# Kernel tuning notes

Hardware: AMD Instinct MI355X
Metric: run time of the kernel (lower is better)

Reference implementation:

```python
import jax, jax.numpy as jnp
import numpy as np

NUM_EXPERTS = 8
TOP_K = 2
N_EMBD = 1024
SEQ = 2048
BATCH = 1
BLOCK = 128
D_FFN = ((4 * N_EMBD // TOP_K) + BLOCK - 1) // BLOCK * BLOCK  # 2048


def setup_inputs() -> dict:
    key = jax.random.key(0)
    k_x, k_r, k_w1, k_w2 = jax.random.split(key, 4)
    x = jax.random.normal(k_x, (BATCH, SEQ, N_EMBD), dtype=jnp.float32)
    # nn.Linear(n_embd, num_experts, bias=False) -> weight [E, D]
    w_router = jax.random.normal(k_r, (NUM_EXPERTS, N_EMBD), dtype=jnp.float32) * 0.02
    # trunc_normal std=0.02 approximated by clipped normal
    w1 = jnp.clip(jax.random.normal(k_w1, (N_EMBD, D_FFN * NUM_EXPERTS), dtype=jnp.float32) * 0.02, -0.06, 0.06)
    w2 = jnp.clip(jax.random.normal(k_w2, (D_FFN * NUM_EXPERTS, N_EMBD), dtype=jnp.float32) * 0.02, -0.06, 0.06)
    return {"x": x, "w_router": w_router, "w1": w1, "w2": w2}


def reference(x, w_router, w1, w2):
    B, S, D = x.shape
    E = w_router.shape[0]
    d_ffn = w1.shape[1] // E
    xf = x.reshape(-1, D)                      # [N, D]
    N = xf.shape[0]

    # --- routing (softmax in fp32, top-k, renormalize) ---
    logits = xf @ w_router.T                   # [N, E]
    probs = jax.nn.softmax(logits.astype(jnp.float32), axis=-1)
    topw, sel = jax.lax.top_k(probs, TOP_K)    # [N, k]
    topw = topw / jnp.sum(topw, axis=-1, keepdims=True)
    topw = topw.astype(x.dtype)

    # dense per-token gate matrix [N, E]; zero for unselected experts, so the
    # dense grouped-GEMM below computes exactly the routed-expert math.
    gates = jnp.zeros((N, E), dtype=x.dtype).at[jnp.arange(N)[:, None], sel].set(topw)

    w1r = w1.reshape(D, E, d_ffn)              # expert e uses columns e*d_ffn:(e+1)*d_ffn
    w2r = w2.reshape(E, d_ffn, D)

    out = jnp.zeros_like(xf)
    for e in range(E):                         # small fixed expert count
        h = jax.nn.gelu(xf @ w1r[:, e, :], approximate=False)  # torch F.gelu = exact erf
        out = out + gates[:, e:e + 1] * (h @ w2r[e])
    return out.reshape(B, S, D)
```

## Files before the change

kernel.cpp:

```cpp
#include <hip/hip_runtime.h>

typedef short bf16x8 __attribute__((ext_vector_type(8)));
typedef float f32x4 __attribute__((ext_vector_type(4)));
typedef unsigned short u16;
typedef unsigned int u32;

#define N_TOK 2048
#define D_EMB 1024
#define D_FFNC 2048
#define N_EXP 8

__device__ __forceinline__ u16 f2bf(float f) {
    u32 u = __builtin_bit_cast(u32, f);
    u32 r = (u + 0x7fffu + ((u >> 16) & 1u)) >> 16;
    return (u16)r;
}

__device__ __forceinline__ void gl_lds16(const void* g, void* l) {
    __builtin_amdgcn_global_load_lds((const __attribute__((address_space(1))) u32*)g,
                                     (__attribute__((address_space(3))) u32*)l, 16, 0, 0);
}

__global__ __launch_bounds__(256) void k_router(const float* __restrict__ x,
                                                const float* __restrict__ wr,
                                                u16* __restrict__ xb,
                                                int* __restrict__ eids,
                                                float* __restrict__ gate2) {
    int lane = threadIdx.x & 63;
    int wv = threadIdx.x >> 6;
    int t = blockIdx.x * 4 + wv;
    const float* xp = x + (size_t)t * D_EMB;
    float p[N_EXP];
#pragma unroll
    for (int e = 0; e < N_EXP; e++) p[e] = 0.f;
#pragma unroll
    for (int i = 0; i < 4; i++) {
        int idx = (i * 64 + lane) * 4;
        float4 v = *reinterpret_cast<const float4*>(xp + idx);
        ushort4 o;
        o.x = f2bf(v.x); o.y = f2bf(v.y); o.z = f2bf(v.z); o.w = f2bf(v.w);
        *reinterpret_cast<ushort4*>(xb + (size_t)t * D_EMB + idx) = o;
#pragma unroll
        for (int e = 0; e < N_EXP; e++) {
            float4 w = *reinterpret_cast<const float4*>(wr + e * D_EMB + idx);
            p[e] += v.x * w.x + v.y * w.y + v.z * w.z + v.w * w.w;
        }
    }
#pragma unroll
    for (int off = 32; off; off >>= 1) {
#pragma unroll
        for (int e = 0; e < N_EXP; e++) p[e] += __shfl_xor(p[e], off);
    }
    float mx = p[0];
#pragma unroll
    for (int e = 1; e < N_EXP; e++) mx = fmaxf(mx, p[e]);
    float pr[N_EXP];
#pragma unroll
    for (int e = 0; e < N_EXP; e++) pr[e] = expf(p[e] - mx);
    int e1 = 0; float v1 = pr[0];
#pragma unroll
    for (int e = 1; e < N_EXP; e++) { if (pr[e] > v1) { v1 = pr[e]; e1 = e; } }
    int e2 = -1; float v2 = -1.f;
#pragma unroll
    for (int e = 0; e < N_EXP; e++) { if (e != e1 && pr[e] > v2) { v2 = pr[e]; e2 = e; } }
    if (lane == 0) {
        float inv = 1.f / (v1 + v2);
        eids[t * 2] = e1; eids[t * 2 + 1] = e2;
        gate2[t * 2] = v1 * inv; gate2[t * 2 + 1] = v2 * inv;
    }
}

__global__ __launch_bounds__(256) void k_transpose(const float* __restrict__ in,
                                                   u16* __restrict__ out, int R, int C) {
    __shared__ float tl[64][65];
    int c0 = blockIdx.x * 64, r0 = blockIdx.y * 64;
    int tid = threadIdx.x;
    int rr = tid >> 4, c4 = (tid & 15) * 4;
#pragma unroll
    for (int i = 0; i < 4; i++) {
        int r = rr + i * 16;
        float4 v = *reinterpret_cast<const float4*>(in + (size_t)(r0 + r) * C + c0 + c4);
        tl[r][c4] = v.x; tl[r][c4 + 1] = v.y; tl[r][c4 + 2] = v.z; tl[r][c4 + 3] = v.w;
    }
    __syncthreads();
    int k4 = (tid & 15) * 4;
#pragma unroll
    for (int i = 0; i < 4; i++) {
        int cc = rr + i * 16;
        ushort4 o;
        o.x = f2bf(tl[k4][cc]); o.y = f2bf(tl[k4 + 1][cc]);
        o.z = f2bf(tl[k4 + 2][cc]); o.w = f2bf(tl[k4 + 3][cc]);
        *reinterpret_cast<ushort4*>(out + (size_t)(c0 + cc) * R + r0 + k4) = o;
    }
}

__global__ __launch_bounds__(256) void k_build(const int* __restrict__ eids,
                                               const float* __restrict__ gate2,
                                               int* __restrict__ cnt, int* __restrict__ basep,
                                               int* __restrict__ rowmeta, float* __restrict__ rowgate) {
    __shared__ int scnt[8], sbase[8], sfill[8];
    int tid = threadIdx.x;
    if (tid < 8) { scnt[tid] = 0; sfill[tid] = 0; }
    __syncthreads();
    for (int t = tid; t < N_TOK; t += 256) {
        atomicAdd(&scnt[eids[2 * t]], 1);
        atomicAdd(&scnt[eids[2 * t + 1]], 1);
    }
    __syncthreads();
    if (tid == 0) { int s = 0; for (int e = 0; e < 8; e++) { sbase[e] = s; s += scnt[e]; } }
    __syncthreads();
    if (tid < 8) { cnt[tid] = scnt[tid]; basep[tid] = sbase[tid]; }
    for (int t = tid; t < N_TOK; t += 256) {
#pragma unroll
        for (int s = 0; s < 2; s++) {
            int e = eids[2 * t + s];
            int pos = atomicAdd(&sfill[e], 1);
            int g = sbase[e] + pos;
            rowmeta[g] = t | (s << 16);
            rowgate[g] = gate2[2 * t + s];
        }
    }
}

__global__ __launch_bounds__(256) void k_gemm1(const u16* __restrict__ xb,
                                               const u16* __restrict__ w1t,
                                               const int* __restrict__ cnt,
                                               const int* __restrict__ basep,
                                               const int* __restrict__ rowmeta,
                                               u16* __restrict__ hbuf) {
    int e = blockIdx.z;
    int nrows = cnt[e];
    int mt = blockIdx.x, nt = blockIdx.y;
    if (mt * 128 >= nrows) return;
    int b0 = basep[e];
    __shared__ u16 lA[128 * 64];
    __shared__ u16 lB[128 * 64];
    int tid = threadIdx.x, lane = tid & 63, wv = tid >> 6;
    int srow8 = lane >> 3;
    int c8 = lane & 7;
    int csw = (c8 ^ srow8) * 16;
    const char* xbB = (const char*)xb;
    const char* w1tB = (const char*)w1t;
    size_t asrc[4], bsrc[4];
    u16 *adst[4], *bdst[4];
#pragma unroll
    for (int i = 0; i < 4; i++) {
        int r = wv * 32 + i * 8 + srow8;
        int g = mt * 128 + r;
        int tok = (g < nrows) ? (rowmeta[b0 + g] & 0xffff) : (rowmeta[b0] & 0xffff);
        asrc[i] = (size_t)tok * 2048 + csw;
        int colg = nt * 128 + r;
        bsrc[i] = (size_t)(e * 2048 + colg) * 2048 + csw;
        adst[i] = lA + (wv * 32 + i * 8) * 64;
        bdst[i] = lB + (wv * 32 + i * 8) * 64;
    }
    f32x4 acc[4][4];
#pragma unroll
    for (int m = 0; m < 4; m++)
#pragma unroll
        for (int n = 0; n < 4; n++) acc[m][n] = (f32x4){0.f, 0.f, 0.f, 0.f};
    int wr = (wv >> 1) * 64, wc = (wv & 1) * 64;
    int lr = lane & 15, kg = lane >> 4;
#pragma unroll
    for (int i = 0; i < 4; i++) { gl_lds16(xbB + asrc[i], adst[i]); gl_lds16(w1tB + bsrc[i], bdst[i]); }
    for (int kt = 0; kt < 16; kt++) {
        __syncthreads();
#pragma unroll
        for (int h2 = 0; h2 < 2; h2++) {
            bf16x8 af[4], bfr[4];
#pragma unroll
            for (int m = 0; m < 4; m++)
                af[m] = *(const bf16x8*)(lA + (wr + m * 16 + lr) * 64 + (((h2 * 4 + kg) ^ (lr & 7)) * 8));
#pragma unroll
            for (int n = 0; n < 4; n++)
                bfr[n] = *(const bf16x8*)(lB + (wc + n * 16 + lr) * 64 + (((h2 * 4 + kg) ^ (lr & 7)) * 8));
#pragma unroll
            for (int m = 0; m < 4; m++)
#pragma unroll
                for (int n = 0; n < 4; n++)
                    acc[m][n] = __builtin_amdgcn_mfma_f32_16x16x32_bf16(af[m], bfr[n], acc[m][n], 0, 0, 0);
        }
        __syncthreads();
        if (kt < 15) {
            size_t ko = (size_t)(kt + 1) * 128;
#pragma unroll
            for (int i = 0; i < 4; i++) { gl_lds16(xbB + asrc[i] + ko, adst[i]); gl_lds16(w1tB + bsrc[i] + ko, bdst[i]); }
        }
    }
#pragma unroll
    for (int m = 0; m < 4; m++) {
        int rbase = wr + m * 16 + kg * 4;
#pragma unroll
        for (int j = 0; j < 4; j++) {
            int r = mt * 128 + rbase + j;
            if (r < nrows) {
                u16* hp = hbuf + (size_t)(b0 + r) * D_FFNC + nt * 128 + wc + lr;
#pragma unroll
                for (int n = 0; n < 4; n++) {
                    float v = acc[m][n][j];
                    v = 0.5f * v * (1.f + erff(v * 0.70710678118654752f));
                    hp[n * 16] = f2bf(v);
                }
            }
        }
    }
}

__global__ __launch_bounds__(256) void k_gemm2(const u16* __restrict__ hbuf,
                                               const u16* __restrict__ w2t,
                                               const int* __restrict__ cnt,
                                               const int* __restrict__ basep,
                                               const int* __restrict__ rowmeta,
                                               const float* __restrict__ rowgate,
                                               float* __restrict__ out2) {
    int e = blockIdx.z;
    int nrows = cnt[e];
    int mt = blockIdx.x, nt = blockIdx.y;
    if (mt * 128 >= nrows) return;
    int b0 = basep[e];
    __shared__ u16 lA[128 * 64];
    __shared__ u16 lB[128 * 64];
    int tid = threadIdx.x, lane = tid & 63, wv = tid >> 6;
    int srow8 = lane >> 3;
    int c8 = lane & 7;
    int csw = (c8 ^ srow8) * 16;
    const char* hB = (const char*)hbuf;
    const char* w2tB = (const char*)w2t;
    size_t asrc[4], bsrc[4];
    u16 *adst[4], *bdst[4];
#pragma unroll
    for (int i = 0; i < 4; i++) {
        int r = wv * 32 + i * 8 + srow8;
        int g = mt * 128 + r;
        int hr = b0 + ((g < nrows) ? g : (nrows - 1));
        asrc[i] = (size_t)hr * 4096 + csw;
        int colg = nt * 128 + r;
        bsrc[i] = (size_t)colg * 32768 + (size_t)e * 4096 + csw;
        adst[i] = lA + (wv * 32 + i * 8) * 64;
        bdst[i] = lB + (wv * 32 + i * 8) * 64;
    }
    f32x4 acc[4][4];
#pragma unroll
    for (int m = 0; m < 4; m++)
#pragma unroll
        for (int n = 0; n < 4; n++) acc[m][n] = (f32x4){0.f, 0.f, 0.f, 0.f};
    int wr = (wv >> 1) * 64, wc = (wv & 1) * 64;
    int lr = lane & 15, kg = lane >> 4;
#pragma unroll
    for (int i = 0; i < 4; i++) { gl_lds16(hB + asrc[i], adst[i]); gl_lds16(w2tB + bsrc[i], bdst[i]); }
    for (int kt = 0; kt < 32; kt++) {
        __syncthreads();
#pragma unroll
        for (int h2 = 0; h2 < 2; h2++) {
            bf16x8 af[4], bfr[4];
#pragma unroll
            for (int m = 0; m < 4; m++)
                af[m] = *(const bf16x8*)(lA + (wr + m * 16 + lr) * 64 + (((h2 * 4 + kg) ^ (lr & 7)) * 8));
#pragma unroll
            for (int n = 0; n < 4; n++)
                bfr[n] = *(const bf16x8*)(lB + (wc + n * 16 + lr) * 64 + (((h2 * 4 + kg) ^ (lr & 7)) * 8));
#pragma unroll
            for (int m = 0; m < 4; m++)
#pragma unroll
                for (int n = 0; n < 4; n++)
                    acc[m][n] = __builtin_amdgcn_mfma_f32_16x16x32_bf16(af[m], bfr[n], acc[m][n], 0, 0, 0);
        }
        __syncthreads();
        if (kt < 31) {
            size_t ko = (size_t)(kt + 1) * 128;
#pragma unroll
            for (int i = 0; i < 4; i++) { gl_lds16(hB + asrc[i] + ko, adst[i]); gl_lds16(w2tB + bsrc[i] + ko, bdst[i]); }
        }
    }
#pragma unroll
    for (int m = 0; m < 4; m++) {
        int rbase = wr + m * 16 + kg * 4;
#pragma unroll
        for (int j = 0; j < 4; j++) {
            int r = mt * 128 + rbase + j;
            if (r < nrows) {
                int meta = rowmeta[b0 + r];
                int tok = meta & 0xffff;
                int slot = meta >> 16;
                float gw = rowgate[b0 + r];
                float* op = out2 + ((size_t)tok * 2 + slot) * D_EMB + nt * 128 + wc + lr;
#pragma unroll
                for (int n = 0; n < 4; n++) op[n * 16] = gw * acc[m][n][j];
            }
        }
    }
}

__global__ __launch_bounds__(256) void k_combine(const float* __restrict__ out2,
                                                 float* __restrict__ out) {
    int idx = blockIdx.x * 256 + threadIdx.x;
    int t = idx >> 8;
    int d4 = (idx & 255) * 4;
    float4 a = *reinterpret_cast<const float4*>(out2 + (size_t)t * 2 * D_EMB + d4);
    float4 b = *reinterpret_cast<const float4*>(out2 + ((size_t)t * 2 + 1) * D_EMB + d4);
    float4 r;
    r.x = a.x + b.x; r.y = a.y + b.y; r.z = a.z + b.z; r.w = a.w + b.w;
    *reinterpret_cast<float4*>(out + (size_t)t * D_EMB + d4) = r;
}

extern "C" void kernel_launch(void* const* d_in, const int* in_sizes, int n_in,
                              void* d_out, int out_size, void* d_ws, size_t ws_size,
                              hipStream_t stream) {
    const float* x = (const float*)d_in[0];
    const float* wrt = (const float*)d_in[1];
    const float* w1 = (const float*)d_in[2];
    const float* w2 = (const float*)d_in[3];
    float* out = (float*)d_out;
    char* ws = (char*)d_ws;
    size_t off = 0;
    auto alloc = [&](size_t b) { void* p = ws + off; off += (b + 255) & ~(size_t)255; return p; };
    u16* xb = (u16*)alloc((size_t)N_TOK * D_EMB * 2);
    u16* w1t = (u16*)alloc((size_t)16384 * 1024 * 2);
    u16* w2t = (u16*)alloc((size_t)16384 * 1024 * 2);
    u16* hbuf = (u16*)alloc((size_t)4096 * D_FFNC * 2);
    float* out2 = (float*)alloc((size_t)N_TOK * 2 * D_EMB * 4);
    int* eids = (int*)alloc(N_TOK * 2 * 4);
    float* gate2 = (float*)alloc(N_TOK * 2 * 4);
    int* rowmeta = (int*)alloc(4096 * 4);
    float* rowgate = (float*)alloc(4096 * 4);
    int* cnt = (int*)alloc(64);
    int* basep = (int*)alloc(64);

    k_router<<<512, 256, 0, stream>>>(x, wrt, xb, eids, gate2);
    k_transpose<<<dim3(256, 16), 256, 0, stream>>>(w1, w1t, 1024, 16384);
    k_transpose<<<dim3(16, 256), 256, 0, stream>>>(w2, w2t, 16384, 1024);
    k_build<<<1, 256, 0, stream>>>(eids, gate2, cnt, basep, rowmeta, rowgate);
    k_gemm1<<<dim3(16, 16, 8), 256, 0, stream>>>(xb, w1t, cnt, basep, rowmeta, hbuf);
    k_gemm2<<<dim3(16, 8, 8), 256, 0, stream>>>(hbuf, w2t, cnt, basep, rowmeta, rowgate, out2);
    k_combine<<<2048, 256, 0, stream>>>(out2, out);
}
```

Before: 344.4 us.

## Double-buffer GEMM LDS tiles, fuse transposes, atomic-accumulate expert outputs

Both expert GEMMs now use two LDS buffers. The next K-tile's global-to-LDS loads are issued before computing on the current tile, with a waitcnt and barrier replacing the old sync-compute-sync-load sequence. The two weight transposes are merged into one launch. k_build uses 1024 threads. The per-slot output buffer and combine kernel are replaced by zeroing the output and atomically adding gated results from gemm2. LDS use doubles per block, which may lower occupancy. The fp32 atomics add contention and make the summation order nondeterministic.

```diff
diff --git a/kernel.cpp b/kernel.cpp
--- a/kernel.cpp
+++ b/kernel.cpp
@@ -70,10 +70,14 @@
     }
 }
 
-__global__ __launch_bounds__(256) void k_transpose(const float* __restrict__ in,
-                                                   u16* __restrict__ out, int R, int C) {
+__global__ __launch_bounds__(256) void k_transpose2(const float* __restrict__ w1,
+                                                    const float* __restrict__ w2,
+                                                    u16* __restrict__ w1t,
+                                                    u16* __restrict__ w2t) {
     __shared__ float tl[64][65];
-    int c0 = blockIdx.x * 64, r0 = blockIdx.y * 64;
+    const float* in; u16* out; int R, C, c0, r0;
+    if (blockIdx.z == 0) { in = w1; out = w1t; R = 1024; C = 16384; c0 = blockIdx.x * 64; r0 = blockIdx.y * 64; }
+    else                 { in = w2; out = w2t; R = 16384; C = 1024; c0 = blockIdx.y * 64; r0 = blockIdx.x * 64; }
     int tid = threadIdx.x;
     int rr = tid >> 4, c4 = (tid & 15) * 4;
 #pragma unroll
@@ -94,15 +98,15 @@
     }
 }
 
-__global__ __launch_bounds__(256) void k_build(const int* __restrict__ eids,
-                                               const float* __restrict__ gate2,
-                                               int* __restrict__ cnt, int* __restrict__ basep,
-                                               int* __restrict__ rowmeta, float* __restrict__ rowgate) {
+__global__ __launch_bounds__(1024) void k_build(const int* __restrict__ eids,
+                                                const float* __restrict__ gate2,
+                                                int* __restrict__ cnt, int* __restrict__ basep,
+                                                int* __restrict__ rowmeta, float* __restrict__ rowgate) {
     __shared__ int scnt[8], sbase[8], sfill[8];
     int tid = threadIdx.x;
     if (tid < 8) { scnt[tid] = 0; sfill[tid] = 0; }
     __syncthreads();
-    for (int t = tid; t < N_TOK; t += 256) {
+    for (int t = tid; t < N_TOK; t += 1024) {
         atomicAdd(&scnt[eids[2 * t]], 1);
         atomicAdd(&scnt[eids[2 * t + 1]], 1);
     }
@@ -110,7 +114,7 @@
     if (tid == 0) { int s = 0; for (int e = 0; e < 8; e++) { sbase[e] = s; s += scnt[e]; } }
     __syncthreads();
     if (tid < 8) { cnt[tid] = scnt[tid]; basep[tid] = sbase[tid]; }
-    for (int t = tid; t < N_TOK; t += 256) {
+    for (int t = tid; t < N_TOK; t += 1024) {
 #pragma unroll
         for (int s = 0; s < 2; s++) {
             int e = eids[2 * t + s];
@@ -120,6 +124,11 @@
             rowgate[g] = gate2[2 * t + s];
         }
     }
+}
+
+__global__ __launch_bounds__(256) void k_zero(float* __restrict__ p) {
+    int idx = blockIdx.x * 256 + threadIdx.x;
+    *reinterpret_cast<float4*>(p + (size_t)idx * 4) = (float4){0.f, 0.f, 0.f, 0.f};
 }
 
 __global__ __launch_bounds__(256) void k_gemm1(const u16* __restrict__ xb,
@@ -133,16 +142,15 @@
     int mt = blockIdx.x, nt = blockIdx.y;
     if (mt * 128 >= nrows) return;
     int b0 = basep[e];
-    __shared__ u16 lA[128 * 64];
-    __shared__ u16 lB[128 * 64];
+    __shared__ u16 lA[2][128 * 64];
+    __shared__ u16 lB[2][128 * 64];
     int tid = threadIdx.x, lane = tid & 63, wv = tid >> 6;
-    int srow8 = lane >> 3;
-    int c8 = lane & 7;
+    int srow8 = lane >> 3, c8 = lane & 7;
     int csw = (c8 ^ srow8) * 16;
     const char* xbB = (const char*)xb;
     const char* w1tB = (const char*)w1t;
     size_t asrc[4], bsrc[4];
-    u16 *adst[4], *bdst[4];
+    int ldso[4];
 #pragma unroll
     for (int i = 0; i < 4; i++) {
         int r = wv * 32 + i * 8 + srow8;
@@ -151,8 +159,7 @@
         asrc[i] = (size_t)tok * 2048 + csw;
         int colg = nt * 128 + r;
         bsrc[i] = (size_t)(e * 2048 + colg) * 2048 + csw;
-        adst[i] = lA + (wv * 32 + i * 8) * 64;
-        bdst[i] = lB + (wv * 32 + i * 8) * 64;
+        ldso[i] = (wv * 32 + i * 8) * 64;
     }
     f32x4 acc[4][4];
 #pragma unroll
@@ -161,31 +168,42 @@
         for (int n = 0; n < 4; n++) acc[m][n] = (f32x4){0.f, 0.f, 0.f, 0.f};
     int wr = (wv >> 1) * 64, wc = (wv & 1) * 64;
     int lr = lane & 15, kg = lane >> 4;
-#pragma unroll
-    for (int i = 0; i < 4; i++) { gl_lds16(xbB + asrc[i], adst[i]); gl_lds16(w1tB + bsrc[i], bdst[i]); }
+
+    auto stage = [&](int buf, int kt) {
+        size_t ko = (size_t)kt * 128;
+#pragma unroll
+        for (int i = 0; i < 4; i++) {
+            gl_lds16(xbB + asrc[i] + ko, lA[buf] + ldso[i]);
+            gl_lds16(w1tB + bsrc[i] + ko, lB[buf] + ldso[i]);
+        }
+    };
+    stage(0, 0);
     for (int kt = 0; kt < 16; kt++) {
-        __syncthreads();
+        if (kt < 15) {
+            stage((kt + 1) & 1, kt + 1);
+            asm volatile("s_waitcnt vmcnt(8)" ::: "memory");
+        } else {
+            asm volatile("s_waitcnt vmcnt(0)" ::: "memory");
+        }
+        __builtin_amdgcn_s_barrier();
+        const u16* la = lA[kt & 1];
+        const u16* lb = lB[kt & 1];
 #pragma unroll
         for (int h2 = 0; h2 < 2; h2++) {
             bf16x8 af[4], bfr[4];
 #pragma unroll
             for (int m = 0; m < 4; m++)
-                af[m] = *(const bf16x8*)(lA + (wr + m * 16 + lr) * 64 + (((h2 * 4 + kg) ^ (lr & 7)) * 8));
+                af[m] = *(const bf16x8*)(la + (wr + m * 16 + lr) * 64 + (((h2 * 4 + kg) ^ (lr & 7)) * 8));
 #pragma unroll
             for (int n = 0; n < 4; n++)
-                bfr[n] = *(const bf16x8*)(lB + (wc + n * 16 + lr) * 64 + (((h2 * 4 + kg) ^ (lr & 7)) * 8));
+                bfr[n] = *(const bf16x8*)(lb + (wc + n * 16 + lr) * 64 + (((h2 * 4 + kg) ^ (lr & 7)) * 8));
 #pragma unroll
             for (int m = 0; m < 4; m++)
 #pragma unroll
                 for (int n = 0; n < 4; n++)
                     acc[m][n] = __builtin_amdgcn_mfma_f32_16x16x32_bf16(af[m], bfr[n], acc[m][n], 0, 0, 0);
         }
-        __syncthreads();
-        if (kt < 15) {
-            size_t ko = (size_t)(kt + 1) * 128;
-#pragma unroll
-            for (int i = 0; i < 4; i++) { gl_lds16(xbB + asrc[i] + ko, adst[i]); gl_lds16(w1tB + bsrc[i] + ko, bdst[i]); }
-        }
+        __builtin_amdgcn_s_barrier();
     }
 #pragma unroll
     for (int m = 0; m < 4; m++) {
@@ -212,22 +230,21 @@
                                                const int* __restrict__ basep,
                                                const int* __restrict__ rowmeta,
                                                const float* __restrict__ rowgate,
-                                               float* __restrict__ out2) {
+                                               float* __restrict__ out) {
     int e = blockIdx.z;
     int nrows = cnt[e];
     int mt = blockIdx.x, nt = blockIdx.y;
     if (mt * 128 >= nrows) return;
     int b0 = basep[e];
-    __shared__ u16 lA[128 * 64];
-    __shared__ u16 lB[128 * 64];
+    __shared__ u16 lA[2][128 * 64];
+    __shared__ u16 lB[2][128 * 64];
     int tid = threadIdx.x, lane = tid & 63, wv = tid >> 6;
-    int srow8 = lane >> 3;
-    int c8 = lane & 7;
+    int srow8 = lane >> 3, c8 = lane & 7;
     int csw = (c8 ^ srow8) * 16;
     const char* hB = (const char*)hbuf;
     const char* w2tB = (const char*)w2t;
     size_t asrc[4], bsrc[4];
-    u16 *adst[4], *bdst[4];
+    int ldso[4];
 #pragma unroll
     for (int i = 0; i < 4; i++) {
         int r = wv * 32 + i * 8 + srow8;
@@ -236,8 +253,7 @@
         asrc[i] = (size_t)hr * 4096 + csw;
         int colg = nt * 128 + r;
         bsrc[i] = (size_t)colg * 32768 + (size_t)e * 4096 + csw;
-        adst[i] = lA + (wv * 32 + i * 8) * 64;
-        bdst[i] = lB + (wv * 32 + i * 8) * 64;
+        ldso[i] = (wv * 32 + i * 8) * 64;
     }
     f32x4 acc[4][4];
 #pragma unroll
@@ -246,31 +262,42 @@
         for (int n = 0; n < 4; n++) acc[m][n] = (f32x4){0.f, 0.f, 0.f, 0.f};
     int wr = (wv >> 1) * 64, wc = (wv & 1) * 64;
     int lr = lane & 15, kg = lane >> 4;
-#pragma unroll
-    for (int i = 0; i < 4; i++) { gl_lds16(hB + asrc[i], adst[i]); gl_lds16(w2tB + bsrc[i], bdst[i]); }
+
+    auto stage = [&](int buf, int kt) {
+        size_t ko = (size_t)kt * 128;
+#pragma unroll
+        for (int i = 0; i < 4; i++) {
+            gl_lds16(hB + asrc[i] + ko, lA[buf] + ldso[i]);
+            gl_lds16(w2tB + bsrc[i] + ko, lB[buf] + ldso[i]);
+        }
+    };
+    stage(0, 0);
     for (int kt = 0; kt < 32; kt++) {
-        __syncthreads();
+        if (kt < 31) {
+            stage((kt + 1) & 1, kt + 1);
+            asm volatile("s_waitcnt vmcnt(8)" ::: "memory");
+        } else {
+            asm volatile("s_waitcnt vmcnt(0)" ::: "memory");
+        }
+        __builtin_amdgcn_s_barrier();
+        const u16* la = lA[kt & 1];
+        const u16* lb = lB[kt & 1];
 #pragma unroll
         for (int h2 = 0; h2 < 2; h2++) {
             bf16x8 af[4], bfr[4];
 #pragma unroll
             for (int m = 0; m < 4; m++)
-                af[m] = *(const bf16x8*)(lA + (wr + m * 16 + lr) * 64 + (((h2 * 4 + kg) ^ (lr & 7)) * 8));
+                af[m] = *(const bf16x8*)(la + (wr + m * 16 + lr) * 64 + (((h2 * 4 + kg) ^ (lr & 7)) * 8));
 #pragma unroll
             for (int n = 0; n < 4; n++)
-                bfr[n] = *(const bf16x8*)(lB + (wc + n * 16 + lr) * 64 + (((h2 * 4 + kg) ^ (lr & 7)) * 8));
+                bfr[n] = *(const bf16x8*)(lb + (wc + n * 16 + lr) * 64 + (((h2 * 4 + kg) ^ (lr & 7)) * 8));
 #pragma unroll
             for (int m = 0; m < 4; m++)
 #pragma unroll
                 for (int n = 0; n < 4; n++)
                     acc[m][n] = __builtin_amdgcn_mfma_f32_16x16x32_bf16(af[m], bfr[n], acc[m][n], 0, 0, 0);
         }
-        __syncthreads();
-        if (kt < 31) {
-            size_t ko = (size_t)(kt + 1) * 128;
-#pragma unroll
-            for (int i = 0; i < 4; i++) { gl_lds16(hB + asrc[i] + ko, adst[i]); gl_lds16(w2tB + bsrc[i] + ko, bdst[i]); }
-        }
+        __builtin_amdgcn_s_barrier();
     }
 #pragma unroll
     for (int m = 0; m < 4; m++) {
@@ -279,28 +306,14 @@
         for (int j = 0; j < 4; j++) {
             int r = mt * 128 + rbase + j;
             if (r < nrows) {
-                int meta = rowmeta[b0 + r];
-                int tok = meta & 0xffff;
-                int slot = meta >> 16;
+                int tok = rowmeta[b0 + r] & 0xffff;
                 float gw = rowgate[b0 + r];
-                float* op = out2 + ((size_t)tok * 2 + slot) * D_EMB + nt * 128 + wc + lr;
-#pragma unroll
-                for (int n = 0; n < 4; n++) op[n * 16] = gw * acc[m][n][j];
+                float* op = out + (size_t)tok * D_EMB + nt * 128 + wc + lr;
+#pragma unroll
+                for (int n = 0; n < 4; n++) atomicAdd(&op[n * 16], gw * acc[m][n][j]);
             }
         }
     }
-}
-
-__global__ __launch_bounds__(256) void k_combine(const float* __restrict__ out2,
-                                                 float* __restrict__ out) {
-    int idx = blockIdx.x * 256 + threadIdx.x;
-    int t = idx >> 8;
-    int d4 = (idx & 255) * 4;
-    float4 a = *reinterpret_cast<const float4*>(out2 + (size_t)t * 2 * D_EMB + d4);
-    float4 b = *reinterpret_cast<const float4*>(out2 + ((size_t)t * 2 + 1) * D_EMB + d4);
-    float4 r;
-    r.x = a.x + b.x; r.y = a.y + b.y; r.z = a.z + b.z; r.w = a.w + b.w;
-    *reinterpret_cast<float4*>(out + (size_t)t * D_EMB + d4) = r;
 }
 
 extern "C" void kernel_launch(void* const* d_in, const int* in_sizes, int n_in,
@@ -318,7 +331,6 @@
     u16* w1t = (u16*)alloc((size_t)16384 * 1024 * 2);
     u16* w2t = (u16*)alloc((size_t)16384 * 1024 * 2);
     u16* hbuf = (u16*)alloc((size_t)4096 * D_FFNC * 2);
-    float* out2 = (float*)alloc((size_t)N_TOK * 2 * D_EMB * 4);
     int* eids = (int*)alloc(N_TOK * 2 * 4);
     float* gate2 = (float*)alloc(N_TOK * 2 * 4);
     int* rowmeta = (int*)alloc(4096 * 4);
@@ -327,10 +339,9 @@
     int* basep = (int*)alloc(64);
 
     k_router<<<512, 256, 0, stream>>>(x, wrt, xb, eids, gate2);
-    k_transpose<<<dim3(256, 16), 256, 0, stream>>>(w1, w1t, 1024, 16384);
-    k_transpose<<<dim3(16, 256), 256, 0, stream>>>(w2, w2t, 16384, 1024);
-    k_build<<<1, 256, 0, stream>>>(eids, gate2, cnt, basep, rowmeta, rowgate);
+    k_transpose2<<<dim3(256, 16, 2), 256, 0, stream>>>(w1, w2, w1t, w2t);
+    k_build<<<1, 1024, 0, stream>>>(eids, gate2, cnt, basep, rowmeta, rowgate);
+    k_zero<<<2048, 256, 0, stream>>>(out);
     k_gemm1<<<dim3(16, 16, 8), 256, 0, stream>>>(xb, w1t, cnt, basep, rowmeta, hbuf);
-    k_gemm2<<<dim3(16, 8, 8), 256, 0, stream>>>(hbuf, w2t, cnt, basep, rowmeta, rowgate, out2);
-    k_combine<<<2048, 256, 0, stream>>>(out2, out);
-}
+    k_gemm2<<<dim3(16, 8, 8), 256, 0, stream>>>(hbuf, w2t, cnt, basep, rowmeta, rowgate, out);
+}
```

Result: slower. 383.4 us (+11.3%).
